# Kernel tuning notes

Measured on AMD Instinct MI355X. Metric: run time of the kernel, lower is better.

The kernel has to match this reference:

```python
import jax, jax.numpy as jnp
import numpy as np

_EPSILON = 1e-06

def _sparsemax(z):
    # sparsemax along last axis (Martins & Astudillo 2016, sort-based projection)
    m = z.shape[-1]
    z_sorted = jnp.flip(jnp.sort(z, axis=-1), axis=-1)          # descending
    z_cum = jnp.cumsum(z_sorted, axis=-1)
    r = jnp.arange(1, m + 1, dtype=z.dtype)
    support = (1.0 + r * z_sorted) > z_cum                       # [b, m]
    k = jnp.sum(support, axis=-1, keepdims=True)                 # support size, int
    tau = (jnp.take_along_axis(z_cum, k - 1, axis=-1) - 1.0) / k.astype(z.dtype)
    return jnp.maximum(z - tau, 0.0)

def setup_inputs() -> dict:
    key = jax.random.key(0)
    ks = jax.random.split(key, 4)
    b, m, d, out = 2048, 8192, 1024, 1000
    encoder_output = jax.random.normal(ks[0], (b, d), dtype=jnp.float32)
    memory_set = jax.random.normal(ks[1], (m, d), dtype=jnp.float32)
    W1 = jax.random.normal(ks[2], (d, 2 * d), dtype=jnp.float32) * (1.0 / np.sqrt(d))
    b1 = jnp.zeros((2 * d,), dtype=jnp.float32)
    W2 = jax.random.normal(ks[3], (2 * d, out), dtype=jnp.float32) * (1.0 / np.sqrt(2 * d))
    b2 = jnp.zeros((out,), dtype=jnp.float32)
    return {"encoder_output": encoder_output, "memory_set": memory_set,
            "W1": W1, "b1": b1, "W2": W2, "b2": b2}

def reference(encoder_output, memory_set, W1, b1, W2, b2):
    # cosine distance: 1 - x_hat @ y_hat^T  (with eps inside the sqrt, as in torch code)
    x_norm = encoder_output / jnp.sqrt(jnp.sum(encoder_output * encoder_output, axis=1, keepdims=True) + _EPSILON)
    y_norm = memory_set / jnp.sqrt(jnp.sum(memory_set * memory_set, axis=1, keepdims=True) + _EPSILON)
    dist = 1.0 - jnp.matmul(x_norm, y_norm.T)                    # [b, m]
    content_weights = _sparsemax(-dist)                          # [b, m]
    memory_vector = jnp.matmul(content_weights, memory_set)      # [b, d]
    h = jax.nn.relu(jnp.matmul(memory_vector, W1) + b1)          # [b, 2d]
    output = jnp.matmul(h, W2) + b2                              # [b, out]
    return output
```

## Files before the change

kernel.cpp:

```cpp
#include <hip/hip_runtime.h>
#include <hip/hip_bf16.h>


#define TPB 256
#define CAP 1024

typedef __bf16 bf16x8 __attribute__((ext_vector_type(8)));
typedef float  f32x4  __attribute__((ext_vector_type(4)));

typedef const __attribute__((address_space(1))) void* gas_ptr;
typedef __attribute__((address_space(3))) void*       las_ptr;

__device__ __forceinline__ unsigned short f2bf(float f) {
    __hip_bfloat16 h = __float2bfloat16(f);
    union { __hip_bfloat16 h; unsigned short s; } u; u.h = h; return u.s;
}
__device__ __forceinline__ float bf2f(unsigned short s) {
    union { unsigned int b; float f; } u; u.b = (unsigned int)s << 16; return u.f;
}
__device__ __forceinline__ unsigned short f2h(float f) {
    union { _Float16 h; unsigned short s; } u; u.h = (_Float16)f; return u.s;
}
__device__ __forceinline__ float h2f(unsigned short s) {
    union { unsigned short s; _Float16 h; } u; u.s = s; return (float)u.h;
}

__device__ __forceinline__ float block_reduce_sum(float v, float* sred) {
    #pragma unroll
    for (int off = 32; off > 0; off >>= 1) v += __shfl_down(v, off, 64);
    int lane = threadIdx.x & 63, wid = threadIdx.x >> 6;
    if (lane == 0) sred[wid] = v;
    __syncthreads();
    if (threadIdx.x == 0) sred[0] = sred[0] + sred[1] + sred[2] + sred[3];
    __syncthreads();
    float r = sred[0];
    __syncthreads();
    return r;
}

__device__ __forceinline__ void block_reduce_sum2(float& a, float& b, float* sred) {
    #pragma unroll
    for (int off = 32; off > 0; off >>= 1) {
        a += __shfl_down(a, off, 64);
        b += __shfl_down(b, off, 64);
    }
    int lane = threadIdx.x & 63, wid = threadIdx.x >> 6;
    if (lane == 0) { sred[wid] = a; sred[4 + wid] = b; }
    __syncthreads();
    if (threadIdx.x == 0) {
        sred[0] = sred[0] + sred[1] + sred[2] + sred[3];
        sred[4] = sred[4] + sred[5] + sred[6] + sred[7];
    }
    __syncthreads();
    a = sred[0]; b = sred[4];
    __syncthreads();
}

__global__ __launch_bounds__(TPB) void normalize_rows_bf16(const float* __restrict__ X0,
                                                           unsigned short* __restrict__ Y0,
                                                           const float* __restrict__ X1,
                                                           unsigned short* __restrict__ Y1,
                                                           float* __restrict__ norms1,
                                                           int nrow0, int cols) {
    __shared__ float sred[4];
    int r = blockIdx.x, tid = threadIdx.x;
    const float* X; unsigned short* Y; float* nn; int row;
    if (r < nrow0) { X = X0; Y = Y0; nn = nullptr; row = r; }
    else           { X = X1; Y = Y1; nn = norms1; row = r - nrow0; }
    const float4* x4 = (const float4*)(X + (size_t)row * cols);
    ushort4* y4 = (ushort4*)(Y + (size_t)row * cols);
    int n4 = cols >> 2;
    float ss = 0.f;
    for (int i = tid; i < n4; i += TPB) {
        float4 v = x4[i];
        ss += v.x * v.x + v.y * v.y + v.z * v.z + v.w * v.w;
    }
    float tot = block_reduce_sum(ss, sred);
    float nrm = sqrtf(tot + 1e-6f);
    float inv = 1.0f / nrm;
    if (nn && tid == 0) nn[row] = nrm;
    for (int i = tid; i < n4; i += TPB) {
        float4 v = x4[i];
        ushort4 o;
        o.x = f2bf(v.x * inv); o.y = f2bf(v.y * inv);
        o.z = f2bf(v.z * inv); o.w = f2bf(v.w * inv);
        y4[i] = o;
    }
}

__device__ __forceinline__ void tc_body(const float* in, unsigned short* out,
                                        int R, int C, int Cpad, int bx, int by) {
    __shared__ float t[32][33];
    int x = threadIdx.x & 31, y = threadIdx.x >> 5;
    int r0 = by * 32, c0 = bx * 32;
    #pragma unroll
    for (int yy = y; yy < 32; yy += 8) {
        int c = c0 + x;
        t[yy][x] = (c < C) ? in[(size_t)(r0 + yy) * C + c] : 0.f;
    }
    __syncthreads();
    #pragma unroll
    for (int yy = y; yy < 32; yy += 8) {
        int c = c0 + yy;
        if (c < Cpad)
            out[(size_t)c * R + r0 + x] = f2bf(t[x][yy]);
    }
}

__global__ __launch_bounds__(TPB) void transpose_cast2(const float* __restrict__ in1,
                                                       unsigned short* __restrict__ out1,
                                                       int R1, int C1, int Cp1,
                                                       const float* __restrict__ in2,
                                                       unsigned short* __restrict__ out2,
                                                       int R2, int C2, int Cp2,
                                                       int nblk1) {
    int bid = blockIdx.x;
    if (bid < nblk1) {
        int nx = Cp1 / 32;
        tc_body(in1, out1, R1, C1, Cp1, bid % nx, bid / nx);
    } else {
        bid -= nblk1;
        int nx = Cp2 / 32;
        tc_body(in2, out2, R2, C2, Cp2, bid % nx, bid / nx);
    }
}

__device__ __forceinline__ void acc8(float* acc, float w, uint4 v) {
    unsigned int ww[4] = {v.x, v.y, v.z, v.w};
    #pragma unroll
    for (int k = 0; k < 4; ++k) {
        acc[2 * k]     += w * bf2f((unsigned short)(ww[k] & 0xffffu));
        acc[2 * k + 1] += w * bf2f((unsigned short)(ww[k] >> 16));
    }
}

__global__ __launch_bounds__(TPB, 8) void sparsemax_gather(const unsigned short* __restrict__ Zh,
                                                           const float* __restrict__ ynorm,
                                                           const unsigned short* __restrict__ yn,
                                                           unsigned short* __restrict__ mv,
                                                           int m, int d) {
    __shared__ float sred[8];
    __shared__ unsigned short cidx[CAP];
    __shared__ float cval[CAP];
    __shared__ unsigned int lcnt;
    constexpr int NR = 4;
    int row = blockIdx.x, tid = threadIdx.x;
    const uint4* zr8 = (const uint4*)(Zh + (size_t)row * m);

    uint4 zreg[NR];
    float s = 0.f, q = 0.f;
    #pragma unroll
    for (int j = 0; j < NR; ++j) {
        uint4 v = zr8[tid + j * TPB];
        zreg[j] = v;
        unsigned int ww[4] = {v.x, v.y, v.z, v.w};
        #pragma unroll
        for (int k = 0; k < 4; ++k) {
            float a = h2f((unsigned short)(ww[k] & 0xffffu));
            float bq = h2f((unsigned short)(ww[k] >> 16));
            s += a + bq; q += a * a + bq * bq;
        }
    }
    if (tid == 0) lcnt = 0;
    block_reduce_sum2(s, q, sred);
    float fm   = (float)m;
    float mean = s / fm;
    float sig  = sqrtf(fmaxf(q / fm - mean * mean, 0.f));
    float tau_s = (s - 1.f) / fm;
    float tau_g = mean + 2.f * sig;

    float Sg = 0.f, cg = 0.f, Ss = 0.f, cs = 0.f;
    #pragma unroll
    for (int j = 0; j < NR; ++j) {
        unsigned int ww[4] = {zreg[j].x, zreg[j].y, zreg[j].z, zreg[j].w};
        #pragma unroll
        for (int k = 0; k < 4; ++k) {
            float a = h2f((unsigned short)(ww[k] & 0xffffu));
            float bq = h2f((unsigned short)(ww[k] >> 16));
            if (a > tau_g) { Sg += a - tau_g; cg += 1.f; }
            if (a > tau_s) { Ss += a - tau_s; cs += 1.f; }
            if (bq > tau_g) { Sg += bq - tau_g; cg += 1.f; }
            if (bq > tau_s) { Ss += bq - tau_s; cs += 1.f; }
        }
    }
    block_reduce_sum2(Sg, cg, sred);
    block_reduce_sum2(Ss, cs, sred);

    float tau_lb, S_act, c_act;
    if (Sg >= 1.f) { tau_lb = tau_g; S_act = Sg + cg * tau_g; c_act = cg; }
    else           { tau_lb = tau_s; S_act = Ss + cs * tau_s; c_act = cs; }
    float tau1 = (S_act - 1.f) / c_act;
    if (tau1 < tau_lb) tau1 = tau_lb;

    #pragma unroll
    for (int j = 0; j < NR; ++j) {
        int base = (tid + j * TPB) * 8;
        unsigned int ww[4] = {zreg[j].x, zreg[j].y, zreg[j].z, zreg[j].w};
        #pragma unroll
        for (int k = 0; k < 4; ++k) {
            float a = h2f((unsigned short)(ww[k] & 0xffffu));
            float bq = h2f((unsigned short)(ww[k] >> 16));
            if (a > tau1) {
                unsigned int slot = atomicAdd(&lcnt, 1u);
                if (slot < CAP) { cidx[slot] = (unsigned short)(base + 2 * k); cval[slot] = a; }
            }
            if (bq > tau1) {
                unsigned int slot = atomicAdd(&lcnt, 1u);
                if (slot < CAP) { cidx[slot] = (unsigned short)(base + 2 * k + 1); cval[slot] = bq; }
            }
        }
    }
    __syncthreads();

    int fast = (lcnt <= CAP && lcnt > 0);
    float tau = tau1;
    int n = (int)lcnt;
    if (fast) {
        if ((tid >> 6) == 0) {
            int lane = tid & 63;
            float tau_l = tau1, prev = -1.f;
            for (int it = 0; it < 64; ++it) {
                float S = 0.f, c = 0.f;
                for (int jj = lane; jj < n; jj += 64) {
                    float z = cval[jj];
                    if (z > tau_l) { S += z; c += 1.f; }
                }
                #pragma unroll
                for (int off = 32; off > 0; off >>= 1) {
                    S += __shfl_down(S, off, 64);
                    c += __shfl_down(c, off, 64);
                }
                S = __shfl(S, 0, 64);
                c = __shfl(c, 0, 64);
                if (c < 0.5f || c == prev) break;
                tau_l = (S - 1.f) / c; prev = c;
            }
            if (lane == 0) sred[0] = tau_l;
        }
        __syncthreads();
        tau = sred[0];
        for (int jj = tid; jj < n; jj += TPB) {
            float w = cval[jj] - tau;
            cval[jj] = (w > 0.f) ? w * ynorm[cidx[jj]] : 0.f;
        }
        __syncthreads();
    } else {
        float prev = -1.f;
        for (int it = 0; it < 64; ++it) {
            float S = 0.f, c = 0.f;
            #pragma unroll
            for (int j = 0; j < NR; ++j) {
                unsigned int ww[4] = {zreg[j].x, zreg[j].y, zreg[j].z, zreg[j].w};
                #pragma unroll
                for (int k = 0; k < 4; ++k) {
                    float a = h2f((unsigned short)(ww[k] & 0xffffu));
                    float bq = h2f((unsigned short)(ww[k] >> 16));
                    if (a > tau) { S += a; c += 1.f; }
                    if (bq > tau) { S += bq; c += 1.f; }
                }
            }
            block_reduce_sum2(S, c, sred);
            if (c < 0.5f || c == prev) break;
            tau = (S - 1.f) / c; prev = c;
        }
    }

    int g = tid >> 7;
    int c0 = (tid & 127) * 8;
    float acc[8] = {};
    if (fast) {
        int j = g;
        for (; j + 6 < n; j += 8) {
            int i0 = cidx[j],     i1 = cidx[j + 2];
            int i2 = cidx[j + 4], i3 = cidx[j + 6];
            float w0 = cval[j],     w1 = cval[j + 2];
            float w2 = cval[j + 4], w3 = cval[j + 6];
            uint4 v0 = *(const uint4*)&yn[(size_t)i0 * d + c0];
            uint4 v1 = *(const uint4*)&yn[(size_t)i1 * d + c0];
            uint4 v2 = *(const uint4*)&yn[(size_t)i2 * d + c0];
            uint4 v3 = *(const uint4*)&yn[(size_t)i3 * d + c0];
            acc8(acc, w0, v0); acc8(acc, w1, v1);
            acc8(acc, w2, v2); acc8(acc, w3, v3);
        }
        for (; j < n; j += 2) {
            float w = cval[j];
            int idx = (int)cidx[j];
            uint4 v = *(const uint4*)&yn[(size_t)idx * d + c0];
            acc8(acc, w, v);
        }
    } else {
        const unsigned short* zrow = Zh + (size_t)row * m;
        for (int i = g; i < m; i += 2) {
            float w = h2f(zrow[i]) - tau;
            if (w <= 0.f) continue;
            w *= ynorm[i];
            uint4 v = *(const uint4*)&yn[(size_t)i * d + c0];
            acc8(acc, w, v);
        }
    }
    __syncthreads();
    float* comb = cval;
    if (g == 1) {
        #pragma unroll
        for (int k = 0; k < 8; ++k) comb[(tid & 127) * 8 + k] = acc[k];
    }
    __syncthreads();
    if (g == 0) {
        #pragma unroll
        for (int k = 0; k < 8; ++k) acc[k] += comb[(tid & 127) * 8 + k];
        unsigned int w0 = f2bf(acc[0]) | ((unsigned int)f2bf(acc[1]) << 16);
        unsigned int w1 = f2bf(acc[2]) | ((unsigned int)f2bf(acc[3]) << 16);
        unsigned int w2 = f2bf(acc[4]) | ((unsigned int)f2bf(acc[5]) << 16);
        unsigned int w3 = f2bf(acc[6]) | ((unsigned int)f2bf(acc[7]) << 16);
        uint4 st = {w0, w1, w2, w3};
        *(uint4*)&mv[(size_t)row * d + c0] = st;
    }
}

template <int BM, int BN, int WM, int WN, int OUTMODE, int RELU, int HASBIAS>
__global__ __launch_bounds__((BM / WM) * (BN / WN) * 64)
void gemm_bt(const unsigned short* __restrict__ A,
             const unsigned short* __restrict__ B,
             const float* __restrict__ bias,
             void* __restrict__ C,
             int M, int K, int lda, int NOUT, int ldc) {
    constexpr int NW   = (BM / WM) * (BN / WN);
    constexpr int TPBL = NW * 64;
    constexpr int ITM  = WM / 16;
    constexpr int ITN  = WN / 16;
    __shared__ unsigned short lA[BM * 64];
    __shared__ unsigned short lB[BN * 64];
    int tid = threadIdx.x;
    int lane = tid & 63, wv = tid >> 6;
    int wm = (wv % (BM / WM)) * WM;
    int wn = (wv / (BM / WM)) * WN;
    int lr = lane & 15, kq = lane >> 4;

    int rowBase = blockIdx.y * BM;
    int colBase = blockIdx.x * BN;

    f32x4 acc[ITM][ITN] = {};

    for (int k0 = 0; k0 < K; k0 += 64) {
        constexpr int AI = BM * 8 / TPBL;
        #pragma unroll
        for (int l = 0; l < AI; ++l) {
            int li = l * TPBL + tid;
            int row = li >> 3, s0 = li & 7;
            int seg = s0 ^ (row & 7);
            const char* gp = (const char*)(A + (size_t)(rowBase + row) * lda + k0) + seg * 16;
            __builtin_amdgcn_global_load_lds((gas_ptr)gp, (las_ptr)((char*)lA + li * 16), 16, 0, 0);
        }
        constexpr int BI = BN * 8 / TPBL;
        #pragma unroll
        for (int l = 0; l < BI; ++l) {
            int li = l * TPBL + tid;
            int row = li >> 3, s0 = li & 7;
            int seg = s0 ^ (row & 7);
            const char* gp = (const char*)(B + (size_t)(colBase + row) * K + k0) + seg * 16;
            __builtin_amdgcn_global_load_lds((gas_ptr)gp, (las_ptr)((char*)lB + li * 16), 16, 0, 0);
        }
        __syncthreads();

        #pragma unroll
        for (int h = 0; h < 2; ++h) {
            bf16x8 av[ITM], bv[ITN];
            #pragma unroll
            for (int i = 0; i < ITM; ++i) {
                int row = wm + i * 16 + lr;
                av[i] = *(const bf16x8*)((const char*)lA + row * 128
                                         + ((((h << 2) | kq) ^ (row & 7)) * 16));
            }
            #pragma unroll
            for (int j = 0; j < ITN; ++j) {
                int row = wn + j * 16 + lr;
                bv[j] = *(const bf16x8*)((const char*)lB + row * 128
                                         + ((((h << 2) | kq) ^ (row & 7)) * 16));
            }
            #pragma unroll
            for (int i = 0; i < ITM; ++i)
                #pragma unroll
                for (int j = 0; j < ITN; ++j)
                    acc[i][j] = __builtin_amdgcn_mfma_f32_16x16x32_bf16(av[i], bv[j], acc[i][j], 0, 0, 0);
        }
        __syncthreads();
    }

    float* Cf = (float*)C;
    unsigned short* Cb = (unsigned short*)C;
    bool fullN = (colBase + BN) <= NOUT;
    #pragma unroll
    for (int j = 0; j < ITN; ++j) {
        int col = colBase + wn + j * 16 + lr;
        float bv_ = (HASBIAS && col < NOUT) ? bias[col] : 0.f;
        #pragma unroll
        for (int i = 0; i < ITM; ++i) {
            #pragma unroll
            for (int r = 0; r < 4; ++r) {
                int row = rowBase + wm + i * 16 + kq * 4 + r;
                float v = acc[i][j][r] + bv_;
                if (RELU) v = fmaxf(v, 0.f);
                if (OUTMODE == 0) {
                    float p = __shfl_xor(v, 1, 64);
                    if (fullN) {
                        if (!(lr & 1)) { float2 st = {v, p}; *(float2*)&Cf[(size_t)row * ldc + col] = st; }
                    } else if (col < NOUT) {
                        Cf[(size_t)row * ldc + col] = v;
                    }
                } else {
                    unsigned int hh = (OUTMODE == 1) ? (unsigned int)f2bf(v) : (unsigned int)f2h(v);
                    unsigned int p1 = (unsigned int)__shfl_xor((int)hh, 1, 64);
                    unsigned int u = (hh & 0xffffu) | (p1 << 16);
                    unsigned int p2 = (unsigned int)__shfl_xor((int)u, 2, 64);
                    if (fullN) {
                        if (!(lr & 3)) { uint2 st = {u, p2}; *(uint2*)&Cb[(size_t)row * ldc + col] = st; }
                    } else if (col < NOUT) {
                        Cb[(size_t)row * ldc + col] = (unsigned short)hh;
                    }
                }
            }
        }
    }
}

extern "C" void kernel_launch(void* const* d_in, const int* in_sizes, int n_in,
                              void* d_out, int out_size, void* d_ws, size_t ws_size,
                              hipStream_t stream) {
    const float* enc = (const float*)d_in[0];
    const float* mem = (const float*)d_in[1];
    const float* W1  = (const float*)d_in[2];
    const float* b1  = (const float*)d_in[3];
    const float* W2  = (const float*)d_in[4];
    const float* b2  = (const float*)d_in[5];

    const int d    = in_sizes[3] / 2;
    const int b    = in_sizes[0] / d;
    const int m    = in_sizes[1] / d;
    const int d2   = in_sizes[3];
    const int outN = in_sizes[5];
    const int outPad = 1024;

    unsigned short* xn    = (unsigned short*)d_ws;
    unsigned short* yn    = xn  + (size_t)b * d;
    float*          ynorm = (float*)(yn + (size_t)m * d);
    unsigned short* W1T   = (unsigned short*)(ynorm + m);
    unsigned short* W2T   = W1T + (size_t)d2 * d;
    unsigned short* Zh    = W2T + (size_t)outPad * d2;
    unsigned short* mv    = Zh + (size_t)b * m;
    unsigned short* h     = mv + (size_t)b * d;

    normalize_rows_bf16<<<b + m, TPB, 0, stream>>>(enc, xn, mem, yn, ynorm, b, d);

    int nblk1 = (d2 / 32) * (d / 32);
    int nblk2 = (outPad / 32) * (d2 / 32);
    transpose_cast2<<<nblk1 + nblk2, TPB, 0, stream>>>(W1, W1T, d, d2, d2,
                                                       W2, W2T, d2, outN, outPad, nblk1);

    gemm_bt<256, 128, 64, 64, 2, 0, 0><<<dim3(m / 128, b / 256), 512, 0, stream>>>(
        xn, yn, nullptr, Zh, b, d, d, m, m);

    sparsemax_gather<<<b, TPB, 0, stream>>>(Zh, ynorm, yn, mv, m, d);

    gemm_bt<128, 128, 64, 64, 1, 1, 1><<<dim3(d2 / 128, b / 128), 256, 0, stream>>>(
        mv, W1T, b1, h, b, d, d, d2, d2);

    gemm_bt<128, 64, 32, 64, 0, 0, 1><<<dim3(outPad / 64, b / 128), 256, 0, stream>>>(
        h, W2T, b2, d_out, b, d2, d2, outN, outN);
}
```

Before: 259.2 us.

## Prefetch gathered memory rows before tau refinement and software-pipeline the gather loop

The sparsemax_gather kernel now issues global loads for the first candidate memory rows before the wave-0 tau refinement, so load latency overlaps the iterative threshold search. The gather loop keeps eight rows in registers and prefetches the next batch while accumulating, with each weight computed inline from the candidate value and a ynorm value cached in LDS at compaction time. Two block reductions are merged into one four-value reduction, and the cross-group combine uses a strided LDS layout to avoid bank conflicts. The trade-off is higher register pressure from eight uint4 buffers, extra LDS for cnorm, and some wasted loads of row 0 for out-of-range slots.

```diff
diff --git a/kernel.cpp b/kernel.cpp
--- a/kernel.cpp
+++ b/kernel.cpp
@@ -53,6 +53,31 @@
     }
     __syncthreads();
     a = sred[0]; b = sred[4];
+    __syncthreads();
+}
+
+__device__ __forceinline__ void block_reduce_sum4(float& a, float& b, float& c, float& d,
+                                                  float* sred) {
+    #pragma unroll
+    for (int off = 32; off > 0; off >>= 1) {
+        a += __shfl_down(a, off, 64);
+        b += __shfl_down(b, off, 64);
+        c += __shfl_down(c, off, 64);
+        d += __shfl_down(d, off, 64);
+    }
+    int lane = threadIdx.x & 63, wid = threadIdx.x >> 6;
+    if (lane == 0) {
+        sred[wid] = a; sred[4 + wid] = b; sred[8 + wid] = c; sred[12 + wid] = d;
+    }
+    __syncthreads();
+    if (threadIdx.x == 0) {
+        sred[0]  = sred[0] + sred[1] + sred[2] + sred[3];
+        sred[4]  = sred[4] + sred[5] + sred[6] + sred[7];
+        sred[8]  = sred[8] + sred[9] + sred[10] + sred[11];
+        sred[12] = sred[12] + sred[13] + sred[14] + sred[15];
+    }
+    __syncthreads();
+    a = sred[0]; b = sred[4]; c = sred[8]; d = sred[12];
     __syncthreads();
 }
 
@@ -139,9 +164,10 @@
                                                            const unsigned short* __restrict__ yn,
                                                            unsigned short* __restrict__ mv,
                                                            int m, int d) {
-    __shared__ float sred[8];
+    __shared__ float sred[16];
     __shared__ unsigned short cidx[CAP];
     __shared__ float cval[CAP];
+    __shared__ float cnorm[CAP];
     __shared__ unsigned int lcnt;
     constexpr int NR = 4;
     int row = blockIdx.x, tid = threadIdx.x;
@@ -183,8 +209,7 @@
             if (bq > tau_s) { Ss += bq - tau_s; cs += 1.f; }
         }
     }
-    block_reduce_sum2(Sg, cg, sred);
-    block_reduce_sum2(Ss, cs, sred);
+    block_reduce_sum4(Sg, cg, Ss, cs, sred);
 
     float tau_lb, S_act, c_act;
     if (Sg >= 1.f) { tau_lb = tau_g; S_act = Sg + cg * tau_g; c_act = cg; }
@@ -202,11 +227,19 @@
             float bq = h2f((unsigned short)(ww[k] >> 16));
             if (a > tau1) {
                 unsigned int slot = atomicAdd(&lcnt, 1u);
-                if (slot < CAP) { cidx[slot] = (unsigned short)(base + 2 * k); cval[slot] = a; }
+                if (slot < CAP) {
+                    int idx = base + 2 * k;
+                    cidx[slot] = (unsigned short)idx; cval[slot] = a;
+                    cnorm[slot] = ynorm[idx];
+                }
             }
             if (bq > tau1) {
                 unsigned int slot = atomicAdd(&lcnt, 1u);
-                if (slot < CAP) { cidx[slot] = (unsigned short)(base + 2 * k + 1); cval[slot] = bq; }
+                if (slot < CAP) {
+                    int idx = base + 2 * k + 1;
+                    cidx[slot] = (unsigned short)idx; cval[slot] = bq;
+                    cnorm[slot] = ynorm[idx];
+                }
             }
         }
     }
@@ -215,7 +248,18 @@
     int fast = (lcnt <= CAP && lcnt > 0);
     float tau = tau1;
     int n = (int)lcnt;
+
+    int g = tid >> 7;
+    int c0 = (tid & 127) * 8;
+    float acc[8] = {};
     if (fast) {
+        uint4 v[8];
+        #pragma unroll
+        for (int t = 0; t < 8; ++t) {
+            int jj = g + 2 * t;
+            int idx = (jj < n) ? (int)cidx[jj] : 0;
+            v[t] = *(const uint4*)&yn[(size_t)idx * d + c0];
+        }
         if ((tid >> 6) == 0) {
             int lane = tid & 63;
             float tau_l = tau1, prev = -1.f;
@@ -239,11 +283,22 @@
         }
         __syncthreads();
         tau = sred[0];
-        for (int jj = tid; jj < n; jj += TPB) {
-            float w = cval[jj] - tau;
-            cval[jj] = (w > 0.f) ? w * ynorm[cidx[jj]] : 0.f;
-        }
-        __syncthreads();
+        for (int j0 = g; j0 < n; j0 += 16) {
+            #pragma unroll
+            for (int t = 0; t < 8; ++t) {
+                int jc = j0 + 2 * t;
+                uint4 cur = v[t];
+                int jn = jc + 16;
+                int idx = (jn < n) ? (int)cidx[jn] : 0;
+                v[t] = *(const uint4*)&yn[(size_t)idx * d + c0];
+                float w = 0.f;
+                if (jc < n) {
+                    w = cval[jc] - tau;
+                    w = (w > 0.f) ? w * cnorm[jc] : 0.f;
+                }
+                acc8(acc, w, cur);
+            }
+        }
     } else {
         float prev = -1.f;
         for (int it = 0; it < 64; ++it) {
@@ -263,32 +318,6 @@
             if (c < 0.5f || c == prev) break;
             tau = (S - 1.f) / c; prev = c;
         }
-    }
-
-    int g = tid >> 7;
-    int c0 = (tid & 127) * 8;
-    float acc[8] = {};
-    if (fast) {
-        int j = g;
-        for (; j + 6 < n; j += 8) {
-            int i0 = cidx[j],     i1 = cidx[j + 2];
-            int i2 = cidx[j + 4], i3 = cidx[j + 6];
-            float w0 = cval[j],     w1 = cval[j + 2];
-            float w2 = cval[j + 4], w3 = cval[j + 6];
-            uint4 v0 = *(const uint4*)&yn[(size_t)i0 * d + c0];
-            uint4 v1 = *(const uint4*)&yn[(size_t)i1 * d + c0];
-            uint4 v2 = *(const uint4*)&yn[(size_t)i2 * d + c0];
-            uint4 v3 = *(const uint4*)&yn[(size_t)i3 * d + c0];
-            acc8(acc, w0, v0); acc8(acc, w1, v1);
-            acc8(acc, w2, v2); acc8(acc, w3, v3);
-        }
-        for (; j < n; j += 2) {
-            float w = cval[j];
-            int idx = (int)cidx[j];
-            uint4 v = *(const uint4*)&yn[(size_t)idx * d + c0];
-            acc8(acc, w, v);
-        }
-    } else {
         const unsigned short* zrow = Zh + (size_t)row * m;
         for (int i = g; i < m; i += 2) {
             float w = h2f(zrow[i]) - tau;
@@ -299,15 +328,15 @@
         }
     }
     __syncthreads();
-    float* comb = cval;
+    int tcol = tid & 127;
     if (g == 1) {
         #pragma unroll
-        for (int k = 0; k < 8; ++k) comb[(tid & 127) * 8 + k] = acc[k];
+        for (int k = 0; k < 8; ++k) cval[k * 128 + tcol] = acc[k];
     }
     __syncthreads();
     if (g == 0) {
         #pragma unroll
-        for (int k = 0; k < 8; ++k) acc[k] += comb[(tid & 127) * 8 + k];
+        for (int k = 0; k < 8; ++k) acc[k] += cval[k * 128 + tcol];
         unsigned int w0 = f2bf(acc[0]) | ((unsigned int)f2bf(acc[1]) << 16);
         unsigned int w1 = f2bf(acc[2]) | ((unsigned int)f2bf(acc[3]) << 16);
         unsigned int w2 = f2bf(acc[4]) | ((unsigned int)f2bf(acc[5]) << 16);
```

Result: slower. 419.6 us (+61.9%).
